# Optimization experiments

Measured on AMD Instinct MI355X. Metric: run time of the kernel, lower is better.

The kernel has to match this reference:

```python
import jax, jax.numpy as jnp
import numpy as np

HID = 10
EPS = 1e-5
B, H, W = 2, 192, 192


def _cbr(x, w, bn):
    # 1x1 conv (channel matmul) -> training-mode BN -> ReLU
    y = jnp.einsum('oc,bchw->bohw', w, x)
    m = y.mean(axis=(0, 2, 3), keepdims=True)
    v = y.var(axis=(0, 2, 3), keepdims=True)
    y = (y - m) * jax.lax.rsqrt(v + EPS)
    y = y * bn[0][None, :, None, None] + bn[1][None, :, None, None]
    return jax.nn.relu(y)


def _forward(xp, xh, xf, p_fea, h_fea, f_fea,
             w_hf1, bn_hf1, w_hf2, bn_hf2,
             w_phu1, bn_phu1, w_phu2, bn_phu2,
             w_phl1, bn_phl1, w_phl2, bn_phl2,
             w_fd1, bn_fd1, w_fd2, bn_fd2,
             w_hd1, bn_hd1, w_hd2, bn_hd2,
             w_fu, bn_fu, w_hu, bn_hu, w_pu, bn_pu):
    h = HID
    xp_l = [xp[:, i] for i in range(7)]   # each [B, h, H, W]
    xh1, xh2 = xh[:, 1], xh[:, 2]
    xf1 = xf[:, 1]
    # Full_Graph: conv_hf(cat(xh_u, xh_l)) + xf
    xf_new = _cbr(_cbr(jnp.concatenate([xh1, xh2], 1), w_hf1, bn_hf1), w_hf2, bn_hf2) + xf1
    # full_update -> split into cls_f=2 chunks (kept concatenated, [B, 2h, H, W])
    xf_upd = _cbr(jnp.concatenate([f_fea, xf_new], 1), w_fu, bn_fu)
    # full_decomp -> xfh_list (cls_h=3 chunks, kept concatenated, [B, 3h, H, W])
    xfh = _cbr(_cbr(jnp.concatenate([h_fea, xf1], 1), w_fd1, bn_fd1), w_fd2, bn_fd2)
    xfh1, xfh2 = xfh[:, h:2 * h], xfh[:, 2 * h:3 * h]
    # Half_upper_Graph (parts 1..4) and Half_lower_Graph (parts 5,6)
    xhu = xh1 + _cbr(_cbr(jnp.concatenate(xp_l[1:5], 1), w_phu1, bn_phu1), w_phu2, bn_phu2) + xfh1
    xhl = xh2 + _cbr(_cbr(jnp.concatenate(xp_l[5:7], 1), w_phl1, bn_phl1), w_phl2, bn_phl2) + xfh2
    # half_update -> cls_h=3 chunks ([B, 3h, H, W])
    xh_upd = _cbr(jnp.concatenate([h_fea, xhu, xhl], 1), w_hu, bn_hu)
    # half_decomp -> xhp_list (cls_p=7 chunks, [B, 7h, H, W])
    xhp = _cbr(_cbr(jnp.concatenate([p_fea, xh1, xh2], 1), w_hd1, bn_hd1), w_hd2, bn_hd2)
    # Part_Graph: xp[j+1] + xhp[j+1]
    xp_new = [xp_l[j + 1] + xhp[:, (j + 1) * h:(j + 2) * h] for j in range(6)]
    # part_update -> cls_p=7 chunks ([B, 7h, H, W])
    xp_upd = _cbr(jnp.concatenate([p_fea] + xp_new, 1), w_pu, bn_pu)
    # outputs (xp_list_new, xh_list_new, xf_list_new, xfh_list, xhp_list) concatenated on channels
    return jnp.concatenate([xp_upd, xh_upd, xf_upd, xfh, xhp], 1)  # [B, 22h, H, W]


_W_SHAPES = {
    'w_hf1': (20, 20), 'w_hf2': (10, 20),
    'w_phu1': (20, 40), 'w_phu2': (10, 20),
    'w_phl1': (20, 20), 'w_phl2': (10, 20),
    'w_fd1': (30, 266), 'w_fd2': (30, 30),
    'w_hd1': (70, 276), 'w_hd2': (70, 70),
    'w_fu': (20, 266), 'w_hu': (30, 276), 'w_pu': (70, 316),
}


def setup_inputs() -> dict:
    key = jax.random.key(0)
    d = {}
    d['xp'] = jax.random.normal(jax.random.fold_in(key, 0), (B, 7, HID, H, W), jnp.float32)
    d['xh'] = jax.random.normal(jax.random.fold_in(key, 1), (B, 3, HID, H, W), jnp.float32)
    d['xf'] = jax.random.normal(jax.random.fold_in(key, 2), (B, 2, HID, H, W), jnp.float32)
    d['p_fea'] = jax.random.normal(jax.random.fold_in(key, 3), (B, 256, H, W), jnp.float32)
    d['h_fea'] = jax.random.normal(jax.random.fold_in(key, 4), (B, 256, H, W), jnp.float32)
    d['f_fea'] = jax.random.normal(jax.random.fold_in(key, 5), (B, 256, H, W), jnp.float32)
    for i, (n, (co, ci)) in enumerate(_W_SHAPES.items()):
        kw = jax.random.fold_in(key, 100 + i)
        d[n] = jax.random.normal(kw, (co, ci), jnp.float32) / np.float32(np.sqrt(ci))
        kb = jax.random.fold_in(key, 200 + i)
        gamma = 1.0 + 0.1 * jax.random.uniform(kb, (co,), jnp.float32)
        beta = 0.1 * jax.random.normal(jax.random.fold_in(key, 300 + i), (co,), jnp.float32)
        d['bn' + n[1:]] = jnp.stack([gamma, beta], 0)
    return d


def reference(xp, xh, xf, p_fea, h_fea, f_fea,
              w_hf1, bn_hf1, w_hf2, bn_hf2,
              w_phu1, bn_phu1, w_phu2, bn_phu2,
              w_phl1, bn_phl1, w_phl2, bn_phl2,
              w_fd1, bn_fd1, w_fd2, bn_fd2,
              w_hd1, bn_hd1, w_hd2, bn_hd2,
              w_fu, bn_fu, w_hu, bn_hu, w_pu, bn_pu):
    return _forward(xp, xh, xf, p_fea, h_fea, f_fea,
                    w_hf1, bn_hf1, w_hf2, bn_hf2,
                    w_phu1, bn_phu1, w_phu2, bn_phu2,
                    w_phl1, bn_phl1, w_phl2, bn_phl2,
                    w_fd1, bn_fd1, w_fd2, bn_fd2,
                    w_hd1, bn_hd1, w_hd2, bn_hd2,
                    w_fu, bn_fu, w_hu, bn_hu, w_pu, bn_pu)
```

## Files before the change

kernel.cpp:

```cpp
#include <hip/hip_runtime.h>

#define HW   36864
#define NPOS 73728
#define EPSV 1e-5f

#define S1_HF1  0
#define S1_FD1  20
#define S1_PHU1 50
#define S1_PHL1 70
#define S1_HD1  90
#define S2_HF2  160
#define S2_FD2  170
#define S2_PHU2 200
#define S2_PHL2 210
#define S2_HD2  220
#define S3_FU   0
#define S3_HU   20
#define S3_PU   50
#define ST3_FU  290
#define ST3_HU  310
#define ST3_PU  340
#define NSLOT 290
#define NSTAT 410
#define L2OFF 160

#define MT 10

__device__ __forceinline__ float4 ld4(const float* p) { return *(const float4*)p; }

__device__ __forceinline__ float4 bnrelu4(float4 v, float sc, float sh) {
    float4 r;
    r.x = fmaf(v.x, sc, sh); r.y = fmaf(v.y, sc, sh);
    r.z = fmaf(v.z, sc, sh); r.w = fmaf(v.w, sc, sh);
    r.x = r.x > 0.f ? r.x : 0.f;
    r.y = r.y > 0.f ? r.y : 0.f;
    r.z = r.z > 0.f ? r.z : 0.f;
    r.w = r.w > 0.f ? r.w : 0.f;
    return r;
}

template<int CIN, int CINP>
__device__ __forceinline__ void stage_w(const float* __restrict__ w, float* wl)
{
    if (CIN == CINP) {
        for (int idx = threadIdx.x; idx < MT * CIN; idx += 256)
            wl[idx] = w[idx];
    } else {
        for (int idx = threadIdx.x; idx < MT * CIN; idx += 256) {
            int o = idx / CIN;
            int c = idx - o * CIN;
            wl[o * CINP + c] = w[idx];
        }
    }
    __syncthreads();
}

__device__ __forceinline__ void fma4x4(float4& a, float4 w, const float4* buf)
{
    a.x = fmaf(w.x, buf[0].x, a.x); a.y = fmaf(w.x, buf[0].y, a.y);
    a.z = fmaf(w.x, buf[0].z, a.z); a.w = fmaf(w.x, buf[0].w, a.w);
    a.x = fmaf(w.y, buf[1].x, a.x); a.y = fmaf(w.y, buf[1].y, a.y);
    a.z = fmaf(w.y, buf[1].z, a.z); a.w = fmaf(w.y, buf[1].w, a.w);
    a.x = fmaf(w.z, buf[2].x, a.x); a.y = fmaf(w.z, buf[2].y, a.y);
    a.z = fmaf(w.z, buf[2].z, a.z); a.w = fmaf(w.z, buf[2].w, a.w);
    a.x = fmaf(w.w, buf[3].x, a.x); a.y = fmaf(w.w, buf[3].y, a.y);
    a.z = fmaf(w.w, buf[3].z, a.z); a.w = fmaf(w.w, buf[3].w, a.w);
}

template<int CIN, int CINP, class F>
__device__ __forceinline__ void conv4(F fetch, const float* wl,
                                      float* __restrict__ y, int p,
                                      float* __restrict__ sumA,
                                      float* __restrict__ sumqA,
                                      int stat0, float* red)
{
    float4 acc[MT];
#pragma unroll
    for (int o = 0; o < MT; ++o) acc[o] = make_float4(0.f, 0.f, 0.f, 0.f);

    constexpr int CHUNK = 8;
    constexpr int MAIN = (CIN / CHUNK) * CHUNK;
    if (MAIN > 0) {
        float4 buf[CHUNK];
#pragma unroll
        for (int i = 0; i < CHUNK; ++i) buf[i] = fetch(i);
#pragma unroll 1
        for (int c0 = CHUNK; c0 < MAIN; c0 += CHUNK) {
            float4 nxt[CHUNK];
#pragma unroll
            for (int i = 0; i < CHUNK; ++i) nxt[i] = fetch(c0 + i);
            const float* wb = wl + (c0 - CHUNK);
#pragma unroll
            for (int o = 0; o < MT; ++o) {
                float4 w0 = ld4(wb + o * CINP);
                float4 w1 = ld4(wb + o * CINP + 4);
                fma4x4(acc[o], w0, buf);
                fma4x4(acc[o], w1, buf + 4);
            }
#pragma unroll
            for (int i = 0; i < CHUNK; ++i) buf[i] = nxt[i];
        }
        const float* wb = wl + (MAIN - CHUNK);
#pragma unroll
        for (int o = 0; o < MT; ++o) {
            float4 w0 = ld4(wb + o * CINP);
            float4 w1 = ld4(wb + o * CINP + 4);
            fma4x4(acc[o], w0, buf);
            fma4x4(acc[o], w1, buf + 4);
        }
    }
    constexpr int REM = CIN - MAIN;
    int ct = MAIN;
    if (REM >= 4) {
        float4 buf4[4];
#pragma unroll
        for (int i = 0; i < 4; ++i) buf4[i] = fetch(ct + i);
#pragma unroll
        for (int o = 0; o < MT; ++o)
            fma4x4(acc[o], ld4(wl + ct + o * CINP), buf4);
        ct += 4;
    }
#pragma unroll
    for (int c = ct; c < CIN; ++c) {
        float4 x = fetch(c);
#pragma unroll
        for (int o = 0; o < MT; ++o) {
            float wv = wl[o * CINP + c];
            acc[o].x = fmaf(wv, x.x, acc[o].x);
            acc[o].y = fmaf(wv, x.y, acc[o].y);
            acc[o].z = fmaf(wv, x.z, acc[o].z);
            acc[o].w = fmaf(wv, x.w, acc[o].w);
        }
    }

#pragma unroll
    for (int o = 0; o < MT; ++o)
        *(float4*)(y + (size_t)o * NPOS + p) = acc[o];

    int lane = threadIdx.x & 63;
    int wv_  = threadIdx.x >> 6;
#pragma unroll
    for (int o = 0; o < MT; ++o) {
        float s = (acc[o].x + acc[o].y) + (acc[o].z + acc[o].w);
        float q = (acc[o].x * acc[o].x + acc[o].y * acc[o].y)
                + (acc[o].z * acc[o].z + acc[o].w * acc[o].w);
#pragma unroll
        for (int i = 1; i < 64; i <<= 1) {
            s += __shfl_xor(s, i, 64);
            q += __shfl_xor(q, i, 64);
        }
        if (lane == 0) {
            red[(wv_ * MT + o) * 2]     = s;
            red[(wv_ * MT + o) * 2 + 1] = q;
        }
    }
    __syncthreads();
    if (threadIdx.x < MT) {
        int o = threadIdx.x;
        float s = 0.f, q = 0.f;
#pragma unroll
        for (int k = 0; k < 4; ++k) {
            s += red[(k * MT + o) * 2];
            q += red[(k * MT + o) * 2 + 1];
        }
        atomicAdd(&sumA[stat0 + o], s);
        atomicAdd(&sumqA[stat0 + o], q);
    }
}

__global__ void __launch_bounds__(256) stage1_kernel(
    const float* __restrict__ xp, const float* __restrict__ xh,
    const float* __restrict__ xf, const float* __restrict__ p_fea,
    const float* __restrict__ h_fea,
    const float* __restrict__ w_hf1, const float* __restrict__ w_fd1,
    const float* __restrict__ w_phu1, const float* __restrict__ w_phl1,
    const float* __restrict__ w_hd1, float* __restrict__ ws)
{
    __shared__ __align__(16) float wlds[MT * 276];
    __shared__ float red[4 * MT * 2];
    int g = blockIdx.x * 256 + threadIdx.x;
    int p = g * 4;
    int b = (p >= HW) ? 1 : 0;
    int s = p - b * HW;
    float* y     = ws;
    float* sumA  = ws + (size_t)NSLOT * NPOS;
    float* sumqA = sumA + NSTAT;
    int yb = blockIdx.y;

    if (yb < 7) {
        int off = yb * MT;
        stage_w<276, 276>(w_hd1 + off * 276, wlds);
        const float* pb = p_fea + (size_t)b * 256 * HW + s;
        const float* xb = xh + ((size_t)b * 30 + 10) * HW + s;
        conv4<276, 276>([&](int c) { return (c < 256) ? ld4(pb + c * HW)
                                                      : ld4(xb + (c - 256) * HW); },
                        wlds, y + (size_t)(S1_HD1 + off) * NPOS, p,
                        sumA, sumqA, S1_HD1 + off, red);
    } else if (yb < 10) {
        int off = (yb - 7) * MT;
        stage_w<266, 268>(w_fd1 + off * 266, wlds);
        const float* hb  = h_fea + (size_t)b * 256 * HW + s;
        const float* xf1 = xf + ((size_t)b * 20 + 10) * HW + s;
        conv4<266, 268>([&](int c) { return (c < 256) ? ld4(hb + c * HW)
                                                      : ld4(xf1 + (c - 256) * HW); },
                        wlds, y + (size_t)(S1_FD1 + off) * NPOS, p,
                        sumA, sumqA, S1_FD1 + off, red);
    } else if (yb < 12) {
        int off = (yb - 10) * MT;
        stage_w<20, 20>(w_hf1 + off * 20, wlds);
        const float* xb = xh + ((size_t)b * 30 + 10) * HW + s;
        conv4<20, 20>([&](int c) { return ld4(xb + c * HW); },
                      wlds, y + (size_t)(S1_HF1 + off) * NPOS, p,
                      sumA, sumqA, S1_HF1 + off, red);
    } else if (yb < 14) {
        int off = (yb - 12) * MT;
        stage_w<40, 40>(w_phu1 + off * 40, wlds);
        const float* xb = xp + ((size_t)b * 70 + 10) * HW + s;
        conv4<40, 40>([&](int c) { return ld4(xb + c * HW); },
                      wlds, y + (size_t)(S1_PHU1 + off) * NPOS, p,
                      sumA, sumqA, S1_PHU1 + off, red);
    } else {
        int off = (yb - 14) * MT;
        stage_w<20, 20>(w_phl1 + off * 20, wlds);
        const float* xb = xp + ((size_t)b * 70 + 50) * HW + s;
        conv4<20, 20>([&](int c) { return ld4(xb + c * HW); },
                      wlds, y + (size_t)(S1_PHL1 + off) * NPOS, p,
                      sumA, sumqA, S1_PHL1 + off, red);
    }
}

__global__ void scale_kernel(int stage,
    const float* __restrict__ bn_hf1, const float* __restrict__ bn_hf2,
    const float* __restrict__ bn_phu1, const float* __restrict__ bn_phu2,
    const float* __restrict__ bn_phl1, const float* __restrict__ bn_phl2,
    const float* __restrict__ bn_fd1, const float* __restrict__ bn_fd2,
    const float* __restrict__ bn_hd1, const float* __restrict__ bn_hd2,
    const float* __restrict__ bn_fu, const float* __restrict__ bn_hu,
    const float* __restrict__ bn_pu, float* __restrict__ ws)
{
    int t = threadIdx.x;
    float* sumA   = ws + (size_t)NSLOT * NPOS;
    float* sumqA  = sumA + NSTAT;
    float* scaleA = sumqA + NSTAT;
    float* shiftA = scaleA + NSTAT;
    int stat, local, co;
    const float* bn;
    if (stage == 1) {
        if (t >= 160) return;
        stat = t;
        if      (t < 20) { bn = bn_hf1;  local = t;      co = 20; }
        else if (t < 50) { bn = bn_fd1;  local = t - 20; co = 30; }
        else if (t < 70) { bn = bn_phu1; local = t - 50; co = 20; }
        else if (t < 90) { bn = bn_phl1; local = t - 70; co = 20; }
        else             { bn = bn_hd1;  local = t - 90; co = 70; }
    } else if (stage == 2) {
        if (t >= 130) return;
        stat = 160 + t;
        if      (t < 10) { bn = bn_hf2;  local = t;      co = 10; }
        else if (t < 40) { bn = bn_fd2;  local = t - 10; co = 30; }
        else if (t < 50) { bn = bn_phu2; local = t - 40; co = 10; }
        else if (t < 60) { bn = bn_phl2; local = t - 50; co = 10; }
        else             { bn = bn_hd2;  local = t - 60; co = 70; }
    } else {
        if (t >= 120) return;
        stat = 290 + t;
        if      (t < 20) { bn = bn_fu; local = t;      co = 20; }
        else if (t < 50) { bn = bn_hu; local = t - 20; co = 30; }
        else             { bn = bn_pu; local = t - 50; co = 70; }
    }
    float n  = (float)NPOS;
    float m  = sumA[stat] / n;
    float v  = sumqA[stat] / n - m * m;
    float g  = bn[local];
    float bt = bn[co + local];
    float sc = g * rsqrtf(v + EPSV);
    scaleA[stat] = sc;
    shiftA[stat] = bt - m * sc;
}

__global__ void __launch_bounds__(256) stage2_kernel(
    const float* __restrict__ w_hf2, const float* __restrict__ w_fd2,
    const float* __restrict__ w_phu2, const float* __restrict__ w_phl2,
    const float* __restrict__ w_hd2, float* __restrict__ ws)
{
    __shared__ __align__(16) float wlds[MT * 72];
    __shared__ float red[4 * MT * 2];
    __shared__ float ssc[160], ssh[160];
    int g = blockIdx.x * 256 + threadIdx.x;
    int p = g * 4;
    float* y     = ws;
    float* sumA  = ws + (size_t)NSLOT * NPOS;
    float* sumqA = sumA + NSTAT;
    const float* scaleA = sumqA + NSTAT;
    const float* shiftA = scaleA + NSTAT;

    for (int i = threadIdx.x; i < 160; i += 256) { ssc[i] = scaleA[i]; ssh[i] = shiftA[i]; }
    int yb = blockIdx.y;

    if (yb < 7) {
        int off = yb * MT;
        stage_w<70, 72>(w_hd2 + off * 70, wlds);
        const float* src = y + (size_t)S1_HD1 * NPOS + p;
        conv4<70, 72>([&](int c) {
            return bnrelu4(ld4(src + (size_t)c * NPOS), ssc[S1_HD1 + c], ssh[S1_HD1 + c]); },
            wlds, y + (size_t)(S2_HD2 + off) * NPOS, p, sumA, sumqA, S2_HD2 + off, red);
    } else if (yb < 10) {
        int off = (yb - 7) * MT;
        stage_w<30, 32>(w_fd2 + off * 30, wlds);
        const float* src = y + (size_t)S1_FD1 * NPOS + p;
        conv4<30, 32>([&](int c) {
            return bnrelu4(ld4(src + (size_t)c * NPOS), ssc[S1_FD1 + c], ssh[S1_FD1 + c]); },
            wlds, y + (size_t)(S2_FD2 + off) * NPOS, p, sumA, sumqA, S2_FD2 + off, red);
    } else if (yb == 10) {
        stage_w<20, 20>(w_hf2, wlds);
        const float* src = y + (size_t)S1_HF1 * NPOS + p;
        conv4<20, 20>([&](int c) {
            return bnrelu4(ld4(src + (size_t)c * NPOS), ssc[S1_HF1 + c], ssh[S1_HF1 + c]); },
            wlds, y + (size_t)S2_HF2 * NPOS, p, sumA, sumqA, S2_HF2, red);
    } else if (yb == 11) {
        stage_w<20, 20>(w_phu2, wlds);
        const float* src = y + (size_t)S1_PHU1 * NPOS + p;
        conv4<20, 20>([&](int c) {
            return bnrelu4(ld4(src + (size_t)c * NPOS), ssc[S1_PHU1 + c], ssh[S1_PHU1 + c]); },
            wlds, y + (size_t)S2_PHU2 * NPOS, p, sumA, sumqA, S2_PHU2, red);
    } else {
        stage_w<20, 20>(w_phl2, wlds);
        const float* src = y + (size_t)S1_PHL1 * NPOS + p;
        conv4<20, 20>([&](int c) {
            return bnrelu4(ld4(src + (size_t)c * NPOS), ssc[S1_PHL1 + c], ssh[S1_PHL1 + c]); },
            wlds, y + (size_t)S2_PHL2 * NPOS, p, sumA, sumqA, S2_PHL2, red);
    }
}

__global__ void __launch_bounds__(256) stage3_kernel(
    const float* __restrict__ xp, const float* __restrict__ xh,
    const float* __restrict__ xf, const float* __restrict__ p_fea,
    const float* __restrict__ h_fea, const float* __restrict__ f_fea,
    const float* __restrict__ w_fu, const float* __restrict__ w_hu,
    const float* __restrict__ w_pu, float* __restrict__ ws)
{
    __shared__ __align__(16) float wlds[MT * 316];
    __shared__ float red[4 * MT * 2];
    __shared__ float ssc[130], ssh[130];
    int g = blockIdx.x * 256 + threadIdx.x;
    int p = g * 4;
    int b = (p >= HW) ? 1 : 0;
    int s = p - b * HW;
    float* y     = ws;
    float* sumA  = ws + (size_t)NSLOT * NPOS;
    float* sumqA = sumA + NSTAT;
    const float* scaleA = sumqA + NSTAT;
    const float* shiftA = scaleA + NSTAT;

    for (int i = threadIdx.x; i < 130; i += 256) {
        ssc[i] = scaleA[L2OFF + i]; ssh[i] = shiftA[L2OFF + i];
    }
    int yb = blockIdx.y;

    if (yb < 7) {
        int off = yb * MT;
        stage_w<316, 316>(w_pu + off * 316, wlds);
        const float* pb   = p_fea + (size_t)b * 256 * HW + s;
        const float* yhd2 = y + (size_t)S2_HD2 * NPOS + p;
        const float* xpb  = xp + ((size_t)b * 70 + 10) * HW + s;
        conv4<316, 316>([&](int c) {
            if (c < 256) return ld4(pb + c * HW);
            int cc = c - 256;
            float4 v = bnrelu4(ld4(yhd2 + (size_t)(10 + cc) * NPOS),
                               ssc[S2_HD2 - L2OFF + 10 + cc], ssh[S2_HD2 - L2OFF + 10 + cc]);
            float4 r0 = ld4(xpb + cc * HW);
            return make_float4(v.x + r0.x, v.y + r0.y, v.z + r0.z, v.w + r0.w); },
            wlds, y + (size_t)(S3_PU + off) * NPOS, p, sumA, sumqA, ST3_PU + off, red);
    } else if (yb < 10) {
        int off = (yb - 7) * MT;
        stage_w<276, 276>(w_hu + off * 276, wlds);
        const float* hb    = h_fea + (size_t)b * 256 * HW + s;
        const float* yphu2 = y + (size_t)S2_PHU2 * NPOS + p;
        const float* yphl2 = y + (size_t)S2_PHL2 * NPOS + p;
        const float* yfd2  = y + (size_t)S2_FD2 * NPOS + p;
        const float* xh1b  = xh + ((size_t)b * 30 + 10) * HW + s;
        conv4<276, 276>([&](int c) {
            if (c < 256) return ld4(hb + c * HW);
            if (c < 266) {
                int cc = c - 256;
                float4 a = bnrelu4(ld4(yphu2 + (size_t)cc * NPOS),
                                   ssc[S2_PHU2 - L2OFF + cc], ssh[S2_PHU2 - L2OFF + cc]);
                float4 f = bnrelu4(ld4(yfd2 + (size_t)(10 + cc) * NPOS),
                                   ssc[S2_FD2 - L2OFF + 10 + cc], ssh[S2_FD2 - L2OFF + 10 + cc]);
                float4 r0 = ld4(xh1b + cc * HW);
                return make_float4(r0.x + a.x + f.x, r0.y + a.y + f.y,
                                   r0.z + a.z + f.z, r0.w + a.w + f.w);
            }
            int cc = c - 266;
            float4 a = bnrelu4(ld4(yphl2 + (size_t)cc * NPOS),
                               ssc[S2_PHL2 - L2OFF + cc], ssh[S2_PHL2 - L2OFF + cc]);
            float4 f = bnrelu4(ld4(yfd2 + (size_t)(20 + cc) * NPOS),
                               ssc[S2_FD2 - L2OFF + 20 + cc], ssh[S2_FD2 - L2OFF + 20 + cc]);
            float4 r0 = ld4(xh1b + (10 + cc) * HW);
            return make_float4(r0.x + a.x + f.x, r0.y + a.y + f.y,
                               r0.z + a.z + f.z, r0.w + a.w + f.w); },
            wlds, y + (size_t)(S3_HU + off) * NPOS, p, sumA, sumqA, ST3_HU + off, red);
    } else {
        int off = (yb - 10) * MT;
        stage_w<266, 268>(w_fu + off * 266, wlds);
        const float* fb   = f_fea + (size_t)b * 256 * HW + s;
        const float* yhf2 = y + (size_t)S2_HF2 * NPOS + p;
        const float* xf1  = xf + ((size_t)b * 20 + 10) * HW + s;
        conv4<266, 268>([&](int c) {
            if (c < 256) return ld4(fb + c * HW);
            int cc = c - 256;
            float4 v = bnrelu4(ld4(yhf2 + (size_t)cc * NPOS),
                               ssc[S2_HF2 - L2OFF + cc], ssh[S2_HF2 - L2OFF + cc]);
            float4 r0 = ld4(xf1 + cc * HW);
            return make_float4(v.x + r0.x, v.y + r0.y, v.z + r0.z, v.w + r0.w); },
            wlds, y + (size_t)(S3_FU + off) * NPOS, p, sumA, sumqA, ST3_FU + off, red);
    }
}

__global__ void __launch_bounds__(256) final_kernel(const float* __restrict__ ws,
                                                    float* __restrict__ out)
{
    int g = blockIdx.x * 256 + threadIdx.x;
    int p = g * 4;
    int c = blockIdx.y;
    const float* sumA   = ws + (size_t)NSLOT * NPOS;
    const float* scaleA = sumA + 2 * NSTAT;
    const float* shiftA = scaleA + NSTAT;
    int slot, stat;
    if      (c < 70)  { slot = S3_PU  + c;         stat = ST3_PU  + c;         }
    else if (c < 100) { slot = S3_HU  + (c - 70);  stat = ST3_HU  + (c - 70);  }
    else if (c < 120) { slot = S3_FU  + (c - 100); stat = ST3_FU  + (c - 100); }
    else if (c < 150) { slot = S2_FD2 + (c - 120); stat = S2_FD2 + (c - 120);  }
    else              { slot = S2_HD2 + (c - 150); stat = S2_HD2 + (c - 150);  }
    float4 v = *(const float4*)(ws + (size_t)slot * NPOS + p);
    float sc = scaleA[stat], sh = shiftA[stat];
    v.x = fmaf(v.x, sc, sh); v.x = v.x > 0.f ? v.x : 0.f;
    v.y = fmaf(v.y, sc, sh); v.y = v.y > 0.f ? v.y : 0.f;
    v.z = fmaf(v.z, sc, sh); v.z = v.z > 0.f ? v.z : 0.f;
    v.w = fmaf(v.w, sc, sh); v.w = v.w > 0.f ? v.w : 0.f;
    int b = (p >= HW) ? 1 : 0;
    int s = p - b * HW;
    *(float4*)(out + ((size_t)b * 220 + c) * HW + s) = v;
}

extern "C" void kernel_launch(void* const* d_in, const int* in_sizes, int n_in,
                              void* d_out, int out_size, void* d_ws, size_t ws_size,
                              hipStream_t stream)
{
    const float* xp     = (const float*)d_in[0];
    const float* xh     = (const float*)d_in[1];
    const float* xf     = (const float*)d_in[2];
    const float* p_fea  = (const float*)d_in[3];
    const float* h_fea  = (const float*)d_in[4];
    const float* f_fea  = (const float*)d_in[5];
    const float* w_hf1  = (const float*)d_in[6];  const float* bn_hf1  = (const float*)d_in[7];
    const float* w_hf2  = (const float*)d_in[8];  const float* bn_hf2  = (const float*)d_in[9];
    const float* w_phu1 = (const float*)d_in[10]; const float* bn_phu1 = (const float*)d_in[11];
    const float* w_phu2 = (const float*)d_in[12]; const float* bn_phu2 = (const float*)d_in[13];
    const float* w_phl1 = (const float*)d_in[14]; const float* bn_phl1 = (const float*)d_in[15];
    const float* w_phl2 = (const float*)d_in[16]; const float* bn_phl2 = (const float*)d_in[17];
    const float* w_fd1  = (const float*)d_in[18]; const float* bn_fd1  = (const float*)d_in[19];
    const float* w_fd2  = (const float*)d_in[20]; const float* bn_fd2  = (const float*)d_in[21];
    const float* w_hd1  = (const float*)d_in[22]; const float* bn_hd1  = (const float*)d_in[23];
    const float* w_hd2  = (const float*)d_in[24]; const float* bn_hd2  = (const float*)d_in[25];
    const float* w_fu   = (const float*)d_in[26]; const float* bn_fu   = (const float*)d_in[27];
    const float* w_hu   = (const float*)d_in[28]; const float* bn_hu   = (const float*)d_in[29];
    const float* w_pu   = (const float*)d_in[30]; const float* bn_pu   = (const float*)d_in[31];

    float* ws  = (float*)d_ws;
    float* out = (float*)d_out;

    size_t need_bytes = ((size_t)NSLOT * NPOS + 4 * NSTAT) * sizeof(float);
    if (ws_size < need_bytes) return;

    hipMemsetAsync(ws + (size_t)NSLOT * NPOS, 0, 2 * NSTAT * sizeof(float), stream);

    dim3 blk(256);
    const int GX = NPOS / 1024;
    stage1_kernel<<<dim3(GX, 16), blk, 0, stream>>>(xp, xh, xf, p_fea, h_fea,
                                                    w_hf1, w_fd1, w_phu1, w_phl1, w_hd1, ws);
    scale_kernel<<<1, 256, 0, stream>>>(1, bn_hf1, bn_hf2, bn_phu1, bn_phu2, bn_phl1, bn_phl2,
                                        bn_fd1, bn_fd2, bn_hd1, bn_hd2, bn_fu, bn_hu, bn_pu, ws);
    stage2_kernel<<<dim3(GX, 13), blk, 0, stream>>>(w_hf2, w_fd2, w_phu2, w_phl2, w_hd2, ws);
    scale_kernel<<<1, 256, 0, stream>>>(2, bn_hf1, bn_hf2, bn_phu1, bn_phu2, bn_phl1, bn_phl2,
                                        bn_fd1, bn_fd2, bn_hd1, bn_hd2, bn_fu, bn_hu, bn_pu, ws);
    stage3_kernel<<<dim3(GX, 12), blk, 0, stream>>>(xp, xh, xf, p_fea, h_fea, f_fea,
                                                    w_fu, w_hu, w_pu, ws);
    scale_kernel<<<1, 256, 0, stream>>>(3, bn_hf1, bn_hf2, bn_phu1, bn_phu2, bn_phl1, bn_phl2,
                                        bn_fd1, bn_fd2, bn_hd1, bn_hd2, bn_fu, bn_hu, bn_pu, ws);
    final_kernel<<<dim3(NPOS / 1024, 220), blk, 0, stream>>>(ws, out);
}
```

Baseline: 604.4 us.

## Stream large-CIN conv inputs through LDS with async global_load_lds triple buffering

```diff
diff --git a/kernel.cpp b/kernel.cpp
--- a/kernel.cpp
+++ b/kernel.cpp
@@ -1,4 +1,5 @@
 #include <hip/hip_runtime.h>
+#include <stdint.h>
 
 #define HW   36864
 #define NPOS 73728
@@ -39,6 +40,18 @@
     return r;
 }
 
+__device__ __forceinline__ float4 add4(float4 a, float4 b) {
+    return make_float4(a.x + b.x, a.y + b.y, a.z + b.z, a.w + b.w);
+}
+
+__device__ __forceinline__ void gld_lds16(const float* g, float* l)
+{
+    __builtin_amdgcn_global_load_lds(
+        (const __attribute__((address_space(1))) uint32_t*)g,
+        (__attribute__((address_space(3))) uint32_t*)l,
+        16, 0, 0);
+}
+
 template<int CIN, int CINP>
 __device__ __forceinline__ void stage_w(const float* __restrict__ w, float* wl)
 {
@@ -67,12 +80,83 @@
     a.z = fmaf(w.w, buf[3].z, a.z); a.w = fmaf(w.w, buf[3].w, a.w);
 }
 
+__device__ __forceinline__ void fma1(float4& a, float w, float4 x)
+{
+    a.x = fmaf(w, x.x, a.x); a.y = fmaf(w, x.y, a.y);
+    a.z = fmaf(w, x.z, a.z); a.w = fmaf(w, x.w, a.w);
+}
+
+__device__ __forceinline__ void finish(float4* acc, float* yo, int p,
+                                       float* sumA, float* sumqA, int stat0,
+                                       float* red)
+{
+#pragma unroll
+    for (int o = 0; o < MT; ++o)
+        *(float4*)(yo + (size_t)o * NPOS + p) = acc[o];
+    int lane = threadIdx.x & 63;
+    int wv_  = threadIdx.x >> 6;
+#pragma unroll
+    for (int o = 0; o < MT; ++o) {
+        float s_ = (acc[o].x + acc[o].y) + (acc[o].z + acc[o].w);
+        float q  = (acc[o].x * acc[o].x + acc[o].y * acc[o].y)
+                 + (acc[o].z * acc[o].z + acc[o].w * acc[o].w);
+#pragma unroll
+        for (int i = 1; i < 64; i <<= 1) {
+            s_ += __shfl_xor(s_, i, 64);
+            q  += __shfl_xor(q, i, 64);
+        }
+        if (lane == 0) {
+            red[(wv_ * MT + o) * 2]     = s_;
+            red[(wv_ * MT + o) * 2 + 1] = q;
+        }
+    }
+    __syncthreads();
+    if (threadIdx.x < MT) {
+        int o = threadIdx.x;
+        float s_ = 0.f, q = 0.f;
+#pragma unroll
+        for (int k = 0; k < 4; ++k) {
+            s_ += red[(k * MT + o) * 2];
+            q  += red[(k * MT + o) * 2 + 1];
+        }
+        atomicAdd(&sumA[stat0 + o], s_);
+        atomicAdd(&sumqA[stat0 + o], q);
+    }
+}
+
+template<int NCHUNK, class GP, class CONS>
+__device__ __forceinline__ void pipe_loop(float* wstage, GP gp, CONS cons)
+{
+    static_assert(NCHUNK >= 2, "pipe_loop needs >=2 chunks");
+#pragma unroll
+    for (int i = 0; i < 4; ++i) gld_lds16(gp(i), wstage + i * 256);
+#pragma unroll
+    for (int i = 0; i < 4; ++i) gld_lds16(gp(4 + i), wstage + 1024 + i * 256);
+    int obuf = 2, cbuf = 0;
+#pragma unroll 1
+    for (int k = 0; k <= NCHUNK - 3; ++k) {
+        asm volatile("s_waitcnt vmcnt(4)" ::: "memory");
+        float* dst = wstage + obuf * 1024;
+        int j0 = (k + 2) * 4;
+#pragma unroll
+        for (int i = 0; i < 4; ++i) gld_lds16(gp(j0 + i), dst + i * 256);
+        cons(k, wstage + cbuf * 1024);
+        obuf = (obuf == 2) ? 0 : obuf + 1;
+        cbuf = (cbuf == 2) ? 0 : cbuf + 1;
+    }
+    asm volatile("s_waitcnt vmcnt(4)" ::: "memory");
+    cons(NCHUNK - 2, wstage + cbuf * 1024);
+    cbuf = (cbuf == 2) ? 0 : cbuf + 1;
+    asm volatile("s_waitcnt vmcnt(0)" ::: "memory");
+    cons(NCHUNK - 1, wstage + cbuf * 1024);
+}
+
 template<int CIN, int CINP, class F>
-__device__ __forceinline__ void conv4(F fetch, const float* wl,
-                                      float* __restrict__ y, int p,
-                                      float* __restrict__ sumA,
-                                      float* __restrict__ sumqA,
-                                      int stat0, float* red)
+__device__ __forceinline__ void conv4s(F fetch, const float* wl,
+                                       float* __restrict__ y, int p,
+                                       float* __restrict__ sumA,
+                                       float* __restrict__ sumqA,
+                                       int stat0, float* red)
 {
     float4 acc[MT];
 #pragma unroll
@@ -92,10 +176,8 @@
             const float* wb = wl + (c0 - CHUNK);
 #pragma unroll
             for (int o = 0; o < MT; ++o) {
-                float4 w0 = ld4(wb + o * CINP);
-                float4 w1 = ld4(wb + o * CINP + 4);
-                fma4x4(acc[o], w0, buf);
-                fma4x4(acc[o], w1, buf + 4);
+                fma4x4(acc[o], ld4(wb + o * CINP), buf);
+                fma4x4(acc[o], ld4(wb + o * CINP + 4), buf + 4);
             }
 #pragma unroll
             for (int i = 0; i < CHUNK; ++i) buf[i] = nxt[i];
@@ -103,10 +185,8 @@
         const float* wb = wl + (MAIN - CHUNK);
 #pragma unroll
         for (int o = 0; o < MT; ++o) {
-            float4 w0 = ld4(wb + o * CINP);
-            float4 w1 = ld4(wb + o * CINP + 4);
-            fma4x4(acc[o], w0, buf);
-            fma4x4(acc[o], w1, buf + 4);
+            fma4x4(acc[o], ld4(wb + o * CINP), buf);
+            fma4x4(acc[o], ld4(wb + o * CINP + 4), buf + 4);
         }
     }
     constexpr int REM = CIN - MAIN;
@@ -124,51 +204,13 @@
     for (int c = ct; c < CIN; ++c) {
         float4 x = fetch(c);
 #pragma unroll
-        for (int o = 0; o < MT; ++o) {
-            float wv = wl[o * CINP + c];
-            acc[o].x = fmaf(wv, x.x, acc[o].x);
-            acc[o].y = fmaf(wv, x.y, acc[o].y);
-            acc[o].z = fmaf(wv, x.z, acc[o].z);
-            acc[o].w = fmaf(wv, x.w, acc[o].w);
-        }
-    }
-
-#pragma unroll
-    for (int o = 0; o < MT; ++o)
-        *(float4*)(y + (size_t)o * NPOS + p) = acc[o];
-
-    int lane = threadIdx.x & 63;
-    int wv_  = threadIdx.x >> 6;
-#pragma unroll
-    for (int o = 0; o < MT; ++o) {
-        float s = (acc[o].x + acc[o].y) + (acc[o].z + acc[o].w);
-        float q = (acc[o].x * acc[o].x + acc[o].y * acc[o].y)
-                + (acc[o].z * acc[o].z + acc[o].w * acc[o].w);
-#pragma unroll
-        for (int i = 1; i < 64; i <<= 1) {
-            s += __shfl_xor(s, i, 64);
-            q += __shfl_xor(q, i, 64);
-        }
-        if (lane == 0) {
-            red[(wv_ * MT + o) * 2]     = s;
-            red[(wv_ * MT + o) * 2 + 1] = q;
-        }
-    }
-    __syncthreads();
-    if (threadIdx.x < MT) {
-        int o = threadIdx.x;
-        float s = 0.f, q = 0.f;
-#pragma unroll
-        for (int k = 0; k < 4; ++k) {
-            s += red[(k * MT + o) * 2];
-            q += red[(k * MT + o) * 2 + 1];
-        }
-        atomicAdd(&sumA[stat0 + o], s);
-        atomicAdd(&sumqA[stat0 + o], q);
-    }
-}
-
-__global__ void __launch_bounds__(256) stage1_kernel(
+        for (int o = 0; o < MT; ++o)
+            fma1(acc[o], wl[o * CINP + c], x);
+    }
+    finish(acc, y, p, sumA, sumqA, stat0, red);
+}
+
+__global__ void __launch_bounds__(256, 2) stage1_kernel(
     const float* __restrict__ xp, const float* __restrict__ xh,
     const float* __restrict__ xf, const float* __restrict__ p_fea,
     const float* __restrict__ h_fea,
@@ -176,6 +218,7 @@
     const float* __restrict__ w_phu1, const float* __restrict__ w_phl1,
     const float* __restrict__ w_hd1, float* __restrict__ ws)
 {
+    __shared__ __align__(16) float stagebuf[4 * 3072];
     __shared__ __align__(16) float wlds[MT * 276];
     __shared__ float red[4 * MT * 2];
     int g = blockIdx.x * 256 + threadIdx.x;
@@ -185,6 +228,8 @@
     float* y     = ws;
     float* sumA  = ws + (size_t)NSLOT * NPOS;
     float* sumqA = sumA + NSTAT;
+    float* wstage = stagebuf + (threadIdx.x >> 6) * 3072;
+    int lane4 = (threadIdx.x & 63) * 4;
     int yb = blockIdx.y;
 
     if (yb < 7) {
@@ -192,40 +237,67 @@
         stage_w<276, 276>(w_hd1 + off * 276, wlds);
         const float* pb = p_fea + (size_t)b * 256 * HW + s;
         const float* xb = xh + ((size_t)b * 30 + 10) * HW + s;
-        conv4<276, 276>([&](int c) { return (c < 256) ? ld4(pb + c * HW)
-                                                      : ld4(xb + (c - 256) * HW); },
-                        wlds, y + (size_t)(S1_HD1 + off) * NPOS, p,
-                        sumA, sumqA, S1_HD1 + off, red);
+        float4 acc[MT];
+#pragma unroll
+        for (int o = 0; o < MT; ++o) acc[o] = make_float4(0.f, 0.f, 0.f, 0.f);
+        auto gp = [&](int j) -> const float* {
+            return (j < 256) ? pb + (size_t)j * HW : xb + (size_t)(j - 256) * HW; };
+        pipe_loop<69>(wstage, gp, [&](int k, float* bb) {
+            float4 xs[4];
+#pragma unroll
+            for (int i = 0; i < 4; ++i) xs[i] = *(float4*)(bb + i * 256 + lane4);
+#pragma unroll
+            for (int o = 0; o < MT; ++o)
+                fma4x4(acc[o], ld4(wlds + o * 276 + k * 4), xs);
+        });
+        finish(acc, y + (size_t)(S1_HD1 + off) * NPOS, p, sumA, sumqA, S1_HD1 + off, red);
     } else if (yb < 10) {
         int off = (yb - 7) * MT;
         stage_w<266, 268>(w_fd1 + off * 266, wlds);
         const float* hb  = h_fea + (size_t)b * 256 * HW + s;
         const float* xf1 = xf + ((size_t)b * 20 + 10) * HW + s;
-        conv4<266, 268>([&](int c) { return (c < 256) ? ld4(hb + c * HW)
-                                                      : ld4(xf1 + (c - 256) * HW); },
-                        wlds, y + (size_t)(S1_FD1 + off) * NPOS, p,
-                        sumA, sumqA, S1_FD1 + off, red);
+        float4 acc[MT];
+#pragma unroll
+        for (int o = 0; o < MT; ++o) acc[o] = make_float4(0.f, 0.f, 0.f, 0.f);
+        auto gp = [&](int j) -> const float* {
+            return (j < 256) ? hb + (size_t)j * HW : xf1 + (size_t)(j - 256) * HW; };
+        pipe_loop<66>(wstage, gp, [&](int k, float* bb) {
+            float4 xs[4];
+#pragma unroll
+            for (int i = 0; i < 4; ++i) xs[i] = *(float4*)(bb + i * 256 + lane4);
+#pragma unroll
+            for (int o = 0; o < MT; ++o)
+                fma4x4(acc[o], ld4(wlds + o * 268 + k * 4), xs);
+        });
+        float4 t0 = ld4(xf1 + (size_t)8 * HW);
+        float4 t1 = ld4(xf1 + (size_t)9 * HW);
+#pragma unroll
+        for (int o = 0; o < MT; ++o) {
+            fma1(acc[o], wlds[o * 268 + 264], t0);
+            fma1(acc[o], wlds[o * 268 + 265], t1);
+        }
+        finish(acc, y + (size_t)(S1_FD1 + off) * NPOS, p, sumA, sumqA, S1_FD1 + off, red);
     } else if (yb < 12) {
         int off = (yb - 10) * MT;
         stage_w<20, 20>(w_hf1 + off * 20, wlds);
         const float* xb = xh + ((size_t)b * 30 + 10) * HW + s;
-        conv4<20, 20>([&](int c) { return ld4(xb + c * HW); },
-                      wlds, y + (size_t)(S1_HF1 + off) * NPOS, p,
-                      sumA, sumqA, S1_HF1 + off, red);
+        conv4s<20, 20>([&](int c) { return ld4(xb + c * HW); },
+                       wlds, y + (size_t)(S1_HF1 + off) * NPOS, p,
+                       sumA, sumqA, S1_HF1 + off, red);
     } else if (yb < 14) {
         int off = (yb - 12) * MT;
         stage_w<40, 40>(w_phu1 + off * 40, wlds);
         const float* xb = xp + ((size_t)b * 70 + 10) * HW + s;
-        conv4<40, 40>([&](int c) { return ld4(xb + c * HW); },
-                      wlds, y + (size_t)(S1_PHU1 + off) * NPOS, p,
-                      sumA, sumqA, S1_PHU1 + off, red);
+        conv4s<40, 40>([&](int c) { return ld4(xb + c * HW); },
+                       wlds, y + (size_t)(S1_PHU1 + off) * NPOS, p,
+                       sumA, sumqA, S1_PHU1 + off, red);
     } else {
         int off = (yb - 14) * MT;
         stage_w<20, 20>(w_phl1 + off * 20, wlds);
         const float* xb = xp + ((size_t)b * 70 + 50) * HW + s;
-        conv4<20, 20>([&](int c) { return ld4(xb + c * HW); },
-                      wlds, y + (size_t)(S1_PHL1 + off) * NPOS, p,
-                      sumA, sumqA, S1_PHL1 + off, red);
+        conv4s<20, 20>([&](int c) { return ld4(xb + c * HW); },
+                       wlds, y + (size_t)(S1_PHL1 + off) * NPOS, p,
+                       sumA, sumqA, S1_PHL1 + off, red);
     }
 }
 
@@ -278,11 +350,12 @@
     shiftA[stat] = bt - m * sc;
 }
 
-__global__ void __launch_bounds__(256) stage2_kernel(
+__global__ void __launch_bounds__(256, 2) stage2_kernel(
     const float* __restrict__ w_hf2, const float* __restrict__ w_fd2,
     const float* __restrict__ w_phu2, const float* __restrict__ w_phl2,
     const float* __restrict__ w_hd2, float* __restrict__ ws)
 {
+    __shared__ __align__(16) float stagebuf[4 * 3072];
     __shared__ __align__(16) float wlds[MT * 72];
     __shared__ float red[4 * MT * 2];
     __shared__ float ssc[160], ssh[160];
@@ -293,6 +366,8 @@
     float* sumqA = sumA + NSTAT;
     const float* scaleA = sumqA + NSTAT;
     const float* shiftA = scaleA + NSTAT;
+    float* wstage = stagebuf + (threadIdx.x >> 6) * 3072;
+    int lane4 = (threadIdx.x & 63) * 4;
 
     for (int i = threadIdx.x; i < 160; i += 256) { ssc[i] = scaleA[i]; ssh[i] = shiftA[i]; }
     int yb = blockIdx.y;
@@ -301,44 +376,66 @@
         int off = yb * MT;
         stage_w<70, 72>(w_hd2 + off * 70, wlds);
         const float* src = y + (size_t)S1_HD1 * NPOS + p;
-        conv4<70, 72>([&](int c) {
-            return bnrelu4(ld4(src + (size_t)c * NPOS), ssc[S1_HD1 + c], ssh[S1_HD1 + c]); },
-            wlds, y + (size_t)(S2_HD2 + off) * NPOS, p, sumA, sumqA, S2_HD2 + off, red);
+        float4 acc[MT];
+#pragma unroll
+        for (int o = 0; o < MT; ++o) acc[o] = make_float4(0.f, 0.f, 0.f, 0.f);
+        auto gp = [&](int j) -> const float* { return src + (size_t)j * NPOS; };
+        pipe_loop<17>(wstage, gp, [&](int k, float* bb) {
+            float4 xs[4];
+#pragma unroll
+            for (int i = 0; i < 4; ++i) {
+                int c = k * 4 + i;
+                float4 v = *(float4*)(bb + i * 256 + lane4);
+                xs[i] = bnrelu4(v, ssc[S1_HD1 + c], ssh[S1_HD1 + c]);
+            }
+#pragma unroll
+            for (int o = 0; o < MT; ++o)
+                fma4x4(acc[o], ld4(wlds + o * 72 + k * 4), xs);
+        });
+        float4 t0 = bnrelu4(ld4(src + (size_t)68 * NPOS), ssc[S1_HD1 + 68], ssh[S1_HD1 + 68]);
+        float4 t1 = bnrelu4(ld4(src + (size_t)69 * NPOS), ssc[S1_HD1 + 69], ssh[S1_HD1 + 69]);
+#pragma unroll
+        for (int o = 0; o < MT; ++o) {
+            fma1(acc[o], wlds[o * 72 + 68], t0);
+            fma1(acc[o], wlds[o * 72 + 69], t1);
+        }
+        finish(acc, y + (size_t)(S2_HD2 + off) * NPOS, p, sumA, sumqA, S2_HD2 + off, red);
     } else if (yb < 10) {
         int off = (yb - 7) * MT;
         stage_w<30, 32>(w_fd2 + off * 30, wlds);
         const float* src = y + (size_t)S1_FD1 * NPOS + p;
-        conv4<30, 32>([&](int c) {
+        conv4s<30, 32>([&](int c) {
             return bnrelu4(ld4(src + (size_t)c * NPOS), ssc[S1_FD1 + c], ssh[S1_FD1 + c]); },
             wlds, y + (size_t)(S2_FD2 + off) * NPOS, p, sumA, sumqA, S2_FD2 + off, red);
     } else if (yb == 10) {
         stage_w<20, 20>(w_hf2, wlds);
         const float* src = y + (size_t)S1_HF1 * NPOS + p;
-        conv4<20, 20>([&](int c) {
+        conv4s<20, 20>([&](int c) {
             return bnrelu4(ld4(src + (size_t)c * NPOS), ssc[S1_HF1 + c], ssh[S1_HF1 + c]); },
             wlds, y + (size_t)S2_HF2 * NPOS, p, sumA, sumqA, S2_HF2, red);
     } else if (yb == 11) {
         stage_w<20, 20>(w_phu2, wlds);
         const float* src = y + (size_t)S1_PHU1 * NPOS + p;
-        conv4<20, 20>([&](int c) {
+        conv4s<20, 20>([&](int c) {
             return bnrelu4(ld4(src + (size_t)c * NPOS), ssc[S1_PHU1 + c], ssh[S1_PHU1 + c]); },
             wlds, y + (size_t)S2_PHU2 * NPOS, p, sumA, sumqA, S2_PHU2, red);
     } else {
         stage_w<20, 20>(w_phl2, wlds);
         const float* src = y + (size_t)S1_PHL1 * NPOS + p;
-        conv4<20, 20>([&](int c) {
+        conv4s<20, 20>([&](int c) {
             return bnrelu4(ld4(src + (size_t)c * NPOS), ssc[S1_PHL1 + c], ssh[S1_PHL1 + c]); },
             wlds, y + (size_t)S2_PHL2 * NPOS, p, sumA, sumqA, S2_PHL2, red);
     }
 }
 
-__global__ void __launch_bounds__(256) stage3_kernel(
+__global__ void __launch_bounds__(256, 2) stage3_kernel(
     const float* __restrict__ xp, const float* __restrict__ xh,
     const float* __restrict__ xf, const float* __restrict__ p_fea,
     const float* __restrict__ h_fea, const float* __restrict__ f_fea,
     const float* __restrict__ w_fu, const float* __restrict__ w_hu,
     const float* __restrict__ w_pu, float* __restrict__ ws)
 {
+    __shared__ __align__(16) float stagebuf[4 * 3072];
     __shared__ __align__(16) float wlds[MT * 316];
     __shared__ float red[4 * MT * 2];
     __shared__ float ssc[130], ssh[130];
@@ -351,6 +448,8 @@
     float* sumqA = sumA + NSTAT;
     const float* scaleA = sumqA + NSTAT;
     const float* shiftA = scaleA + NSTAT;
+    float* wstage = stagebuf + (threadIdx.x >> 6) * 3072;
+    int lane4 = (threadIdx.x & 63) * 4;
 
     for (int i = threadIdx.x; i < 130; i += 256) {
         ssc[i] = scaleA[L2OFF + i]; ssh[i] = shiftA[L2OFF + i];
@@ -363,14 +462,41 @@
         const float* pb   = p_fea + (size_t)b * 256 * HW + s;
         const float* yhd2 = y + (size_t)S2_HD2 * NPOS + p;
         const float* xpb  = xp + ((size_t)b * 70 + 10) * HW + s;
-        conv4<316, 316>([&](int c) {
-            if (c < 256) return ld4(pb + c * HW);
-            int cc = c - 256;
-            float4 v = bnrelu4(ld4(yhd2 + (size_t)(10 + cc) * NPOS),
-                               ssc[S2_HD2 - L2OFF + 10 + cc], ssh[S2_HD2 - L2OFF + 10 + cc]);
-            float4 r0 = ld4(xpb + cc * HW);
-            return make_float4(v.x + r0.x, v.y + r0.y, v.z + r0.z, v.w + r0.w); },
-            wlds, y + (size_t)(S3_PU + off) * NPOS, p, sumA, sumqA, ST3_PU + off, red);
+        float4 acc[MT];
+#pragma unroll
+        for (int o = 0; o < MT; ++o) acc[o] = make_float4(0.f, 0.f, 0.f, 0.f);
+        auto gp = [&](int j) -> const float* {
+            if (j < 256) return pb + (size_t)j * HW;
+            int jj = j - 256, t = jj >> 1;
+            return (jj & 1) ? xpb + (size_t)t * HW
+                            : yhd2 + (size_t)(10 + t) * NPOS; };
+        pipe_loop<94>(wstage, gp, [&](int k, float* bb) {
+            if (k < 64) {
+                float4 xs[4];
+#pragma unroll
+                for (int i = 0; i < 4; ++i) xs[i] = *(float4*)(bb + i * 256 + lane4);
+#pragma unroll
+                for (int o = 0; o < MT; ++o)
+                    fma4x4(acc[o], ld4(wlds + o * 316 + k * 4), xs);
+            } else {
+                int t0 = (k - 64) * 2;
+                float4 a0 = *(float4*)(bb + 0 * 256 + lane4);
+                float4 b0 = *(float4*)(bb + 1 * 256 + lane4);
+                float4 a1 = *(float4*)(bb + 2 * 256 + lane4);
+                float4 b1 = *(float4*)(bb + 3 * 256 + lane4);
+                int i0 = S2_HD2 - L2OFF + 10 + t0;
+                float4 x0 = add4(bnrelu4(a0, ssc[i0], ssh[i0]), b0);
+                float4 x1 = add4(bnrelu4(a1, ssc[i0 + 1], ssh[i0 + 1]), b1);
+                int c0 = 256 + t0;
+#pragma unroll
+                for (int o = 0; o < MT; ++o) {
+                    float2 w2 = *(const float2*)(wlds + o * 316 + c0);
+                    fma1(acc[o], w2.x, x0);
+                    fma1(acc[o], w2.y, x1);
+                }
+            }
+        });
+        finish(acc, y + (size_t)(S3_PU + off) * NPOS, p, sumA, sumqA, ST3_PU + off, red);
     } else if (yb < 10) {
         int off = (yb - 7) * MT;
         stage_w<276, 276>(w_hu + off * 276, wlds);
@@ -379,41 +505,83 @@
         const float* yphl2 = y + (size_t)S2_PHL2 * NPOS + p;
         const float* yfd2  = y + (size_t)S2_FD2 * NPOS + p;
         const float* xh1b  = xh + ((size_t)b * 30 + 10) * HW + s;
-        conv4<276, 276>([&](int c) {
-            if (c < 256) return ld4(hb + c * HW);
-            if (c < 266) {
-                int cc = c - 256;
-                float4 a = bnrelu4(ld4(yphu2 + (size_t)cc * NPOS),
-                                   ssc[S2_PHU2 - L2OFF + cc], ssh[S2_PHU2 - L2OFF + cc]);
-                float4 f = bnrelu4(ld4(yfd2 + (size_t)(10 + cc) * NPOS),
-                                   ssc[S2_FD2 - L2OFF + 10 + cc], ssh[S2_FD2 - L2OFF + 10 + cc]);
-                float4 r0 = ld4(xh1b + cc * HW);
-                return make_float4(r0.x + a.x + f.x, r0.y + a.y + f.y,
-                                   r0.z + a.z + f.z, r0.w + a.w + f.w);
+        float4 acc[MT];
+#pragma unroll
+        for (int o = 0; o < MT; ++o) acc[o] = make_float4(0.f, 0.f, 0.f, 0.f);
+        auto gp = [&](int j) -> const float* {
+            if (j < 256) return hb + (size_t)j * HW;
+            int jj = j - 256, t = jj >> 2, r = jj & 3;
+            if (r == 0) return (t < 10) ? yphu2 + (size_t)t * NPOS
+                                        : yphl2 + (size_t)(t - 10) * NPOS;
+            if (r == 1) return yfd2 + (size_t)(10 + t) * NPOS;
+            return xh1b + (size_t)t * HW;
+        };
+        pipe_loop<84>(wstage, gp, [&](int k, float* bb) {
+            if (k < 64) {
+                float4 xs[4];
+#pragma unroll
+                for (int i = 0; i < 4; ++i) xs[i] = *(float4*)(bb + i * 256 + lane4);
+#pragma unroll
+                for (int o = 0; o < MT; ++o)
+                    fma4x4(acc[o], ld4(wlds + o * 276 + k * 4), xs);
+            } else {
+                int t = k - 64, c = 256 + t;
+                float4 A = *(float4*)(bb + 0 * 256 + lane4);
+                float4 F = *(float4*)(bb + 1 * 256 + lane4);
+                float4 R = *(float4*)(bb + 2 * 256 + lane4);
+                int ia = (t < 10) ? (S2_PHU2 - L2OFF + t) : (S2_PHL2 - L2OFF + t - 10);
+                int iff = S2_FD2 - L2OFF + 10 + t;
+                float4 a = bnrelu4(A, ssc[ia], ssh[ia]);
+                float4 f = bnrelu4(F, ssc[iff], ssh[iff]);
+                float4 x = make_float4(R.x + a.x + f.x, R.y + a.y + f.y,
+                                       R.z + a.z + f.z, R.w + a.w + f.w);
+#pragma unroll
+                for (int o = 0; o < MT; ++o)
+                    fma1(acc[o], wlds[o * 276 + c], x);
             }
-            int cc = c - 266;
-            float4 a = bnrelu4(ld4(yphl2 + (size_t)cc * NPOS),
-                               ssc[S2_PHL2 - L2OFF + cc], ssh[S2_PHL2 - L2OFF + cc]);
-            float4 f = bnrelu4(ld4(yfd2 + (size_t)(20 + cc) * NPOS),
-                               ssc[S2_FD2 - L2OFF + 20 + cc], ssh[S2_FD2 - L2OFF + 20 + cc]);
-            float4 r0 = ld4(xh1b + (10 + cc) * HW);
-            return make_float4(r0.x + a.x + f.x, r0.y + a.y + f.y,
-                               r0.z + a.z + f.z, r0.w + a.w + f.w); },
-            wlds, y + (size_t)(S3_HU + off) * NPOS, p, sumA, sumqA, ST3_HU + off, red);
+        });
+        finish(acc, y + (size_t)(S3_HU + off) * NPOS, p, sumA, sumqA, ST3_HU + off, red);
     } else {
         int off = (yb - 10) * MT;
         stage_w<266, 268>(w_fu + off * 266, wlds);
         const float* fb   = f_fea + (size_t)b * 256 * HW + s;
         const float* yhf2 = y + (size_t)S2_HF2 * NPOS + p;
         const float* xf1  = xf + ((size_t)b * 20 + 10) * HW + s;
-        conv4<266, 268>([&](int c) {
-            if (c < 256) return ld4(fb + c * HW);
-            int cc = c - 256;
-            float4 v = bnrelu4(ld4(yhf2 + (size_t)cc * NPOS),
-                               ssc[S2_HF2 - L2OFF + cc], ssh[S2_HF2 - L2OFF + cc]);
-            float4 r0 = ld4(xf1 + cc * HW);
-            return make_float4(v.x + r0.x, v.y + r0.y, v.z + r0.z, v.w + r0.w); },
-            wlds, y + (size_t)(S3_FU + off) * NPOS, p, sumA, sumqA, ST3_FU + off, red);
+        float4 acc[MT];
+#pragma unroll
+        for (int o = 0; o < MT; ++o) acc[o] = make_float4(0.f, 0.f, 0.f, 0.f);
+        auto gp = [&](int j) -> const float* {
+            if (j < 256) return fb + (size_t)j * HW;
+            int jj = j - 256, t = jj >> 1;
+            return (jj & 1) ? xf1 + (size_t)t * HW
+                            : yhf2 + (size_t)t * NPOS; };
+        pipe_loop<69>(wstage, gp, [&](int k, float* bb) {
+            if (k < 64) {
+                float4 xs[4];
+#pragma unroll
+                for (int i = 0; i < 4; ++i) xs[i] = *(float4*)(bb + i * 256 + lane4);
+#pragma unroll
+                for (int o = 0; o < MT; ++o)
+                    fma4x4(acc[o], ld4(wlds + o * 268 + k * 4), xs);
+            } else {
+                int t0 = (k - 64) * 2;
+                float4 a0 = *(float4*)(bb + 0 * 256 + lane4);
+                float4 b0 = *(float4*)(bb + 1 * 256 + lane4);
+                float4 a1 = *(float4*)(bb + 2 * 256 + lane4);
+                float4 b1 = *(float4*)(bb + 3 * 256 + lane4);
+                int i0 = S2_HF2 - L2OFF + t0;
+                float4 x0 = add4(bnrelu4(a0, ssc[i0], ssh[i0]), b0);
+                float4 x1 = add4(bnrelu4(a1, ssc[i0 + 1], ssh[i0 + 1]), b1);
+                int c0 = 256 + t0;
+#pragma unroll
+                for (int o = 0; o < MT; ++o) {
+                    float2 w2 = *(const float2*)(wlds + o * 268 + c0);
+                    fma1(acc[o], w2.x, x0);
+                    fma1(acc[o], w2.y, x1);
+                }
+            }
+        });
+        finish(acc, y + (size_t)(S3_FU + off) * NPOS, p, sumA, sumqA, ST3_FU + off, red);
     }
 }
 
```

New measurement: 635.1 us. 5.1% more time.
